# Optimization experiments

Hardware: AMD Instinct MI355X
Metric: run time of the kernel (lower is better)

## Reference

```python
import jax, jax.numpy as jnp
import numpy as np

D_MODEL = 1024
NUM_HEADS = 16
EPS = 1e-5


def _layernorm(x, gamma, beta):
    mu = jnp.mean(x, axis=-1, keepdims=True)
    var = jnp.mean(jnp.square(x - mu), axis=-1, keepdims=True)
    return (x - mu) * jax.lax.rsqrt(var + EPS) * gamma + beta


def setup_inputs() -> dict:
    key = jax.random.key(0)
    ks = jax.random.split(key, 8)
    B, S, D = 4, 2048, D_MODEL
    xav = (6.0 / (D + D)) ** 0.5  # xavier_uniform bound for square D x D
    inp = {
        "q": jax.random.normal(ks[0], (B, S, D), dtype=jnp.float32),
        "k": jax.random.normal(ks[1], (B, S, D), dtype=jnp.float32),
        "v": jax.random.normal(ks[2], (B, S, D), dtype=jnp.float32),
        "Wq": jax.random.uniform(ks[3], (D, D), jnp.float32, -xav, xav),
        "Wk": jax.random.uniform(ks[4], (D, D), jnp.float32, -xav, xav),
        "Wv": jax.random.uniform(ks[5], (D, D), jnp.float32, -xav, xav),
        "Wo": jax.random.uniform(ks[6], (D, D), jnp.float32, -xav, xav),
        "bo": jnp.zeros((D,), jnp.float32),
        "q_gamma": jnp.ones((D,), jnp.float32),
        "q_beta": jnp.zeros((D,), jnp.float32),
        "k_gamma": jnp.ones((D,), jnp.float32),
        "k_beta": jnp.zeros((D,), jnp.float32),
    }
    return inp


def reference(q, k, v, Wq, Wk, Wv, Wo, bo, q_gamma, q_beta, k_gamma, k_beta):
    B, S, D = q.shape
    H = NUM_HEADS
    scale = 1.0 / (D ** 0.5)  # NOTE: 1/sqrt(d_model), as in the source
    qp = _layernorm(q @ Wq, q_gamma, q_beta)  # LN over full d_model, pre-split
    kp = _layernorm(k @ Wk, k_gamma, k_beta)
    vp = v @ Wv
    qh = qp.reshape(B, S, H, D // H)  # [B,S,H,hd]
    kh = kp.reshape(B, S, H, D // H)
    vh = vp.reshape(B, S, H, D // H)
    attn = jnp.einsum("bqhd,bkhd->bhqk", qh, kh) * scale
    attn = jax.nn.softmax(attn, axis=-1)
    x = jnp.einsum("bhqk,bkhd->bqhd", attn, vh).reshape(B, S, D)
    return x @ Wo + bo
```

## Files before the change

kernel.cpp:

```cpp
#include <hip/hip_runtime.h>
#include <hip/hip_bf16.h>

typedef unsigned short u16;
typedef __attribute__((ext_vector_type(8))) short bf16x8;
typedef __attribute__((ext_vector_type(4))) float f32x4;
typedef __attribute__((ext_vector_type(16))) float f32x16;
typedef __attribute__((ext_vector_type(4))) unsigned short u16x4;
typedef __attribute__((ext_vector_type(4))) unsigned int u32x4;
typedef __attribute__((ext_vector_type(2))) int i32x2;

__device__ __forceinline__ u16 f2b(float f) {
    __hip_bfloat16 h = __float2bfloat16(f);
    u16 r; __builtin_memcpy(&r, &h, 2); return r;
}
__device__ __forceinline__ float bf2f(u16 u) {
    return __uint_as_float(((unsigned)u) << 16);
}
__device__ __forceinline__ void gload16(const void* g, void* l) {
    __builtin_amdgcn_global_load_lds(
        (const __attribute__((address_space(1))) unsigned int*)g,
        (__attribute__((address_space(3))) unsigned int*)l, 16, 0, 0);
}
__device__ __forceinline__ float fexp2(float x) {
    return __builtin_amdgcn_exp2f(x);
}
__device__ __forceinline__ unsigned cvtpk(float lo, float hi) {
    unsigned d;
    asm("v_cvt_pk_bf16_f32 %0, %1, %2" : "=v"(d) : "v"(lo), "v"(hi));
    return d;
}
__device__ __forceinline__ bf16x8 mk_pa(float a0, float a1, float a2, float a3,
                                        float b0, float b1, float b2, float b3) {
    int A0 = (int)cvtpk(a0, a1), A1 = (int)cvtpk(a2, a3);
    int B0 = (int)cvtpk(b0, b1), B1 = (int)cvtpk(b2, b3);
    i32x2 r0 = __builtin_amdgcn_permlane32_swap(A0, B0, false, false);
    i32x2 r1 = __builtin_amdgcn_permlane32_swap(A1, B1, false, false);
    u32x4 fw = { (unsigned)r0[0], (unsigned)r1[0], (unsigned)r0[1], (unsigned)r1[1] };
    return __builtin_bit_cast(bf16x8, fw);
}

__global__ __launch_bounds__(256)
void cvt_kernel(const float* __restrict__ in, u16* __restrict__ out) {
    size_t i = ((size_t)blockIdx.x * 256 + threadIdx.x) * 8;
    f32x4 a = *(const f32x4*)(in + i);
    f32x4 b = *(const f32x4*)(in + i + 4);
    u16x4 p0 = { f2b(a[0]), f2b(a[1]), f2b(a[2]), f2b(a[3]) };
    u16x4 p1 = { f2b(b[0]), f2b(b[1]), f2b(b[2]), f2b(b[3]) };
    *(u16x4*)(out + i) = p0;
    *(u16x4*)(out + i + 4) = p1;
}

__global__ __launch_bounds__(256)
void wt_kernel(const float* __restrict__ Wq, const float* __restrict__ Wk,
               const float* __restrict__ Wv, const float* __restrict__ Wo,
               u16* __restrict__ Wt) {
    const float* W = blockIdx.z == 0 ? Wq : blockIdx.z == 1 ? Wk : blockIdx.z == 2 ? Wv : Wo;
    u16* Out = Wt + (size_t)blockIdx.z * (1024 * 1024);
    __shared__ float T[64][65];
    const int t = threadIdx.x;
    const int r0 = blockIdx.y * 64, c0 = blockIdx.x * 64;
#pragma unroll
    for (int e = 0; e < 4; ++e) {
        int row = e * 16 + (t >> 4), c4 = (t & 15) * 4;
        f32x4 v = *(const f32x4*)(W + (r0 + row) * 1024 + c0 + c4);
        T[row][c4] = v[0]; T[row][c4 + 1] = v[1]; T[row][c4 + 2] = v[2]; T[row][c4 + 3] = v[3];
    }
    __syncthreads();
#pragma unroll
    for (int e = 0; e < 4; ++e) {
        int orow = e * 16 + (t >> 4), oc4 = (t & 15) * 4;
        u16x4 pk = { f2b(T[oc4][orow]), f2b(T[oc4 + 1][orow]),
                     f2b(T[oc4 + 2][orow]), f2b(T[oc4 + 3][orow]) };
        *(u16x4*)(Out + (c0 + orow) * 1024 + r0 + oc4) = pk;
    }
}

template <int BIAS>
__global__ __launch_bounds__(256)
void gemm_kernel(const u16* __restrict__ Ab, const u16* __restrict__ Bt,
                 u16* __restrict__ Cb, float* __restrict__ Cf,
                 const float* __restrict__ bias) {
    constexpr int K = 1024;
    __shared__ u16 As[128 * 64];
    __shared__ u16 Bs[128 * 64];
    const int tid = threadIdx.x;
    const int lane = tid & 63, w = tid >> 6;
    const int wr = w >> 1, wc = w & 1;
    const int c = lane & 15, g = lane >> 4;
    const int m0 = blockIdx.y * 128, n0 = blockIdx.x * 128;
    const int sr = lane >> 3, sc = (lane & 7) * 8;
    f32x4 acc[4][4] = {};
    for (int kt = 0; kt < 16; ++kt) {
        const int k0 = kt * 64;
#pragma unroll
        for (int i = 0; i < 4; ++i) {
            int row = 32 * w + 8 * i;
            gload16(Ab + (size_t)(m0 + row + sr) * K + k0 + sc, &As[row * 64]);
            gload16(Bt + (size_t)(n0 + row + sr) * K + k0 + sc, &Bs[row * 64]);
        }
        __syncthreads();
#pragma unroll
        for (int kk = 0; kk < 2; ++kk) {
            bf16x8 af[4], bfr[4];
#pragma unroll
            for (int m = 0; m < 4; ++m)
                af[m] = *(const bf16x8*)&As[(wr * 64 + m * 16 + c) * 64 + kk * 32 + 8 * g];
#pragma unroll
            for (int n = 0; n < 4; ++n)
                bfr[n] = *(const bf16x8*)&Bs[(wc * 64 + n * 16 + c) * 64 + kk * 32 + 8 * g];
#pragma unroll
            for (int m = 0; m < 4; ++m)
#pragma unroll
                for (int n = 0; n < 4; ++n)
                    acc[m][n] = __builtin_amdgcn_mfma_f32_16x16x32_bf16(af[m], bfr[n], acc[m][n], 0, 0, 0);
        }
        __syncthreads();
    }
#pragma unroll
    for (int n = 0; n < 4; ++n) {
        int col = n0 + wc * 64 + n * 16 + c;
        float bv = BIAS ? bias[col] : 0.0f;
#pragma unroll
        for (int m = 0; m < 4; ++m) {
            int row0 = m0 + wr * 64 + m * 16 + 4 * g;
#pragma unroll
            for (int r = 0; r < 4; ++r) {
                if (BIAS) Cf[(row0 + r) * 1024 + col] = acc[m][n][r] + bv;
                else      Cb[(row0 + r) * 1024 + col] = f2b(acc[m][n][r]);
            }
        }
    }
}

__global__ __launch_bounds__(256)
void ln_kernel(const u16* __restrict__ P, const float* __restrict__ gamma,
               const float* __restrict__ beta, float mul, u16* __restrict__ Out) {
    const int row = blockIdx.x;
    const int tid = threadIdx.x;
    const int lane = tid & 63, w = tid >> 6;
    u16x4 xr = *(const u16x4*)(P + row * 1024 + tid * 4);
    float x0 = bf2f(xr[0]), x1 = bf2f(xr[1]), x2 = bf2f(xr[2]), x3 = bf2f(xr[3]);
    float s = x0 + x1 + x2 + x3;
    float sq = x0 * x0 + x1 * x1 + x2 * x2 + x3 * x3;
#pragma unroll
    for (int m = 1; m < 64; m <<= 1) { s += __shfl_xor(s, m); sq += __shfl_xor(sq, m); }
    __shared__ float red[8];
    if (lane == 0) { red[w] = s; red[4 + w] = sq; }
    __syncthreads();
    float st = red[0] + red[1] + red[2] + red[3];
    float sqt = red[4] + red[5] + red[6] + red[7];
    float mu = st * (1.0f / 1024.0f);
    float var = sqt * (1.0f / 1024.0f) - mu * mu;
    float rs = rsqrtf(var + 1e-5f);
    f32x4 gm = *(const f32x4*)(gamma + tid * 4);
    f32x4 bt = *(const f32x4*)(beta + tid * 4);
    float xs[4] = {x0, x1, x2, x3};
    u16x4 pk;
#pragma unroll
    for (int j = 0; j < 4; ++j)
        pk[j] = f2b(((xs[j] - mu) * rs * gm[j] + bt[j]) * mul);
    const int b = row >> 11, sI = row & 2047;
    const int col = tid * 4, hh = col >> 6, d = col & 63;
    *(u16x4*)(Out + (((b * 16 + hh) * 2048 + sI) << 6) + d) = pk;
}

__global__ __launch_bounds__(256)
void vt_kernel(const u16* __restrict__ P, u16* __restrict__ Vt) {
    __shared__ u16 T[64][72];
    const int t = threadIdx.x;
    const int bh = blockIdx.y, s0 = blockIdx.x * 64;
    const int b = bh >> 4, h = bh & 15;
#pragma unroll
    for (int e = 0; e < 4; ++e) {
        int row = e * 16 + (t >> 4), c4 = (t & 15) * 4;
        u16x4 v = *(const u16x4*)(P + (b * 2048 + s0 + row) * 1024 + h * 64 + c4);
        *(u16x4*)&T[row][c4] = v;
    }
    __syncthreads();
#pragma unroll
    for (int e = 0; e < 4; ++e) {
        int dd = e * 16 + (t >> 4), s4 = (t & 15) * 4;
        u16x4 pk = { T[s4][dd], T[s4 + 1][dd], T[s4 + 2][dd], T[s4 + 3][dd] };
        *(u16x4*)(Vt + ((size_t)bh * 64 + dd) * 2048 + s0 + s4) = pk;
    }
}

__global__ __launch_bounds__(256, 4)
void attn_kernel(const u16* __restrict__ Qa, const u16* __restrict__ Ka,
                 const u16* __restrict__ Vt, u16* __restrict__ Xa) {
    __shared__ u16 Ks[2][4096];
    __shared__ u16 Vs[2][4096];
    const int tid = threadIdx.x;
    const int lane = tid & 63, w = tid >> 6;
    const int col = lane & 31, h = lane >> 5;
    const int bid = blockIdx.x;
    const int bh = (bid & 7) * 8 + ((bid >> 3) & 7);
    const int q0 = (bid >> 6) * 128;
    const int b = bh >> 4, hd = bh & 15;
    const int qb = q0 + w * 32;
    const int sw = (col & 7) << 4;

    const u16* qptr = Qa + ((size_t)bh * 2048 + qb + col) * 64;
    bf16x8 qf[4];
#pragma unroll
    for (int s = 0; s < 4; ++s)
        qf[s] = *(const bf16x8*)(qptr + 16 * s + 8 * h);

    const int sr = lane >> 3;
    const int scg = ((lane & 7) ^ sr) * 8;
    const u16* kA = Ka + ((size_t)bh * 2048 + sr) * 64 + scg;
    const u16* vA = Vt + ((size_t)bh * 64 + sr) * 2048 + scg;

    f32x16 o0 = {}, o1 = {};
    float li = 0.f;

#pragma unroll
    for (int j = 0; j < 2; ++j) {
        const int m = 2 * w + j;
        gload16(kA + (size_t)(8 * m) * 64, &Ks[0][8 * m * 64]);
        gload16(vA + (size_t)(8 * m) * 2048, &Vs[0][8 * m * 64]);
    }
    __syncthreads();

    int cur = 0;
    for (int t = 0; t < 32; ++t) {
        const int tn = (t + 1) & 31;
#pragma unroll
        for (int j = 0; j < 2; ++j) {
            const int m = 2 * w + j;
            gload16(kA + (size_t)(tn * 64 + 8 * m) * 64, &Ks[cur ^ 1][8 * m * 64]);
            gload16(vA + (size_t)(8 * m) * 2048 + tn * 64, &Vs[cur ^ 1][8 * m * 64]);
        }

        const char* kbase = (const char*)&Ks[cur][0];
        f32x16 sacc0 = {}, sacc1 = {};
        __builtin_amdgcn_s_setprio(1);
#pragma unroll
        for (int s = 0; s < 4; ++s) {
            bf16x8 kf0 = *(const bf16x8*)(kbase + (col) * 128       + ((32 * s + 16 * h) ^ sw));
            bf16x8 kf1 = *(const bf16x8*)(kbase + (32 + col) * 128  + ((32 * s + 16 * h) ^ sw));
            sacc0 = __builtin_amdgcn_mfma_f32_32x32x16_bf16(kf0, qf[s], sacc0, 0, 0, 0);
            sacc1 = __builtin_amdgcn_mfma_f32_32x32x16_bf16(kf1, qf[s], sacc1, 0, 0, 0);
        }
        __builtin_amdgcn_s_setprio(0);

        f32x16 p0, p1;
#pragma unroll
        for (int r = 0; r < 16; ++r) { p0[r] = fexp2(sacc0[r]); }
#pragma unroll
        for (int r = 0; r < 16; ++r) { p1[r] = fexp2(sacc1[r]); }
#pragma unroll
        for (int r = 0; r < 16; ++r) { li += p0[r] + p1[r]; }

        bf16x8 pa0 = mk_pa(p0[0], p0[1], p0[2], p0[3], p0[4], p0[5], p0[6], p0[7]);
        bf16x8 pa1 = mk_pa(p0[8], p0[9], p0[10], p0[11], p0[12], p0[13], p0[14], p0[15]);
        bf16x8 pa2 = mk_pa(p1[0], p1[1], p1[2], p1[3], p1[4], p1[5], p1[6], p1[7]);
        bf16x8 pa3 = mk_pa(p1[8], p1[9], p1[10], p1[11], p1[12], p1[13], p1[14], p1[15]);

        const char* vb = (const char*)&Vs[cur][0];
        __builtin_amdgcn_s_setprio(1);
#pragma unroll
        for (int sg = 0; sg < 4; ++sg) {
            bf16x8 pf = sg == 0 ? pa0 : sg == 1 ? pa1 : sg == 2 ? pa2 : pa3;
            const int cb = (32 * sg + 16 * h) ^ sw;
            bf16x8 vf0 = *(const bf16x8*)(vb + (col) * 128      + cb);
            bf16x8 vf1 = *(const bf16x8*)(vb + (32 + col) * 128 + cb);
            o0 = __builtin_amdgcn_mfma_f32_32x32x16_bf16(pf, vf0, o0, 0, 0, 0);
            o1 = __builtin_amdgcn_mfma_f32_32x32x16_bf16(pf, vf1, o1, 0, 0, 0);
        }
        __builtin_amdgcn_s_setprio(0);

        __syncthreads();
        cur ^= 1;
    }

    li += __shfl_xor(li, 32);
    float inv = 1.0f / li;
#pragma unroll
    for (int reg = 0; reg < 16; ++reg) {
        const int crow = (reg & 3) + 8 * (reg >> 2) + 4 * h;
        float ivr = __shfl(inv, crow);
        const int row = qb + crow;
        u16* xp = Xa + ((size_t)b * 2048 + row) * 1024 + hd * 64;
        xp[col] = f2b(o0[reg] * ivr);
        xp[32 + col] = f2b(o1[reg] * ivr);
    }
}

extern "C" void kernel_launch(void* const* d_in, const int* in_sizes, int n_in,
                              void* d_out, int out_size, void* d_ws, size_t ws_size,
                              hipStream_t stream) {
    const float* q   = (const float*)d_in[0];
    const float* k   = (const float*)d_in[1];
    const float* v   = (const float*)d_in[2];
    const float* Wq  = (const float*)d_in[3];
    const float* Wk  = (const float*)d_in[4];
    const float* Wv  = (const float*)d_in[5];
    const float* Wo  = (const float*)d_in[6];
    const float* bo  = (const float*)d_in[7];
    const float* qg  = (const float*)d_in[8];
    const float* qbt = (const float*)d_in[9];
    const float* kg  = (const float*)d_in[10];
    const float* kbt = (const float*)d_in[11];

    char* ws = (char*)d_ws;
    u16* Wt = (u16*)(ws);
    u16* Pb = (u16*)(ws + 8388608);
    u16* Qa = (u16*)(ws + 25165824);
    u16* Ka = (u16*)(ws + 41943040);
    u16* Vt = (u16*)(ws + 58720256);
    u16* Ib = (u16*)(ws + 75497472);
    u16* Xa = Pb;

    const float MUL_Q = 0.04508422002778f;

    wt_kernel<<<dim3(16, 16, 4), 256, 0, stream>>>(Wq, Wk, Wv, Wo, Wt);

    cvt_kernel<<<4096, 256, 0, stream>>>(q, Ib);
    gemm_kernel<0><<<dim3(8, 64), 256, 0, stream>>>(Ib, Wt, Pb, nullptr, nullptr);
    ln_kernel<<<8192, 256, 0, stream>>>(Pb, qg, qbt, MUL_Q, Qa);

    cvt_kernel<<<4096, 256, 0, stream>>>(k, Ib);
    gemm_kernel<0><<<dim3(8, 64), 256, 0, stream>>>(Ib, Wt + 1048576, Pb, nullptr, nullptr);
    ln_kernel<<<8192, 256, 0, stream>>>(Pb, kg, kbt, 1.0f, Ka);

    cvt_kernel<<<4096, 256, 0, stream>>>(v, Ib);
    gemm_kernel<0><<<dim3(8, 64), 256, 0, stream>>>(Ib, Wt + 2097152, Pb, nullptr, nullptr);
    vt_kernel<<<dim3(32, 64), 256, 0, stream>>>(Pb, Vt);

    attn_kernel<<<1024, 256, 0, stream>>>(Qa, Ka, Vt, Xa);

    gemm_kernel<1><<<dim3(8, 64), 256, 0, stream>>>((const u16*)Xa, Wt + 3145728, nullptr, (float*)d_out, bo);
}
```

Measured before the change: 253.7 us.

## Batch Q/K/V conversion, projection GEMMs and layernorms into grid-z launches

Merges the three per-input convert, projection GEMM and layernorm launches into single launches indexed by blockIdx.z, using a larger workspace so all three projections live in separate buffers. Each projection GEMM grid alone is 512 blocks, which may underfill the GPU; a combined 1536-block grid fills more compute units and removes several launch gaps. It needs more workspace and keeps the old sequential path as a fallback when the workspace is too small.

```diff
diff --git a/kernel.cpp b/kernel.cpp
--- a/kernel.cpp
+++ b/kernel.cpp
@@ -51,6 +51,21 @@
 }
 
 __global__ __launch_bounds__(256)
+void cvt3_kernel(const float* __restrict__ q, const float* __restrict__ k,
+                 const float* __restrict__ v, u16* __restrict__ out3) {
+    const int z = blockIdx.z;
+    const float* in = z == 0 ? q : z == 1 ? k : v;
+    u16* out = out3 + (size_t)z * 8388608;
+    size_t i = ((size_t)blockIdx.x * 256 + threadIdx.x) * 8;
+    f32x4 a = *(const f32x4*)(in + i);
+    f32x4 b = *(const f32x4*)(in + i + 4);
+    u16x4 p0 = { f2b(a[0]), f2b(a[1]), f2b(a[2]), f2b(a[3]) };
+    u16x4 p1 = { f2b(b[0]), f2b(b[1]), f2b(b[2]), f2b(b[3]) };
+    *(u16x4*)(out + i) = p0;
+    *(u16x4*)(out + i + 4) = p1;
+}
+
+__global__ __launch_bounds__(256)
 void wt_kernel(const float* __restrict__ Wq, const float* __restrict__ Wk,
                const float* __restrict__ Wv, const float* __restrict__ Wo,
                u16* __restrict__ Wt) {
@@ -76,18 +91,17 @@
 }
 
 template <int BIAS>
-__global__ __launch_bounds__(256)
-void gemm_kernel(const u16* __restrict__ Ab, const u16* __restrict__ Bt,
-                 u16* __restrict__ Cb, float* __restrict__ Cf,
-                 const float* __restrict__ bias) {
+__device__ __forceinline__ void gemm_body(const u16* __restrict__ Ab,
+                                          const u16* __restrict__ Bt,
+                                          u16* __restrict__ Cb, float* __restrict__ Cf,
+                                          const float* __restrict__ bias,
+                                          u16* As, u16* Bs, int bx, int by) {
     constexpr int K = 1024;
-    __shared__ u16 As[128 * 64];
-    __shared__ u16 Bs[128 * 64];
     const int tid = threadIdx.x;
     const int lane = tid & 63, w = tid >> 6;
     const int wr = w >> 1, wc = w & 1;
     const int c = lane & 15, g = lane >> 4;
-    const int m0 = blockIdx.y * 128, n0 = blockIdx.x * 128;
+    const int m0 = by * 128, n0 = bx * 128;
     const int sr = lane >> 3, sc = (lane & 7) * 8;
     f32x4 acc[4][4] = {};
     for (int kt = 0; kt < 16; ++kt) {
@@ -132,9 +146,31 @@
     }
 }
 
-__global__ __launch_bounds__(256)
-void ln_kernel(const u16* __restrict__ P, const float* __restrict__ gamma,
-               const float* __restrict__ beta, float mul, u16* __restrict__ Out) {
+template <int BIAS>
+__global__ __launch_bounds__(256)
+void gemm_kernel(const u16* __restrict__ Ab, const u16* __restrict__ Bt,
+                 u16* __restrict__ Cb, float* __restrict__ Cf,
+                 const float* __restrict__ bias) {
+    __shared__ u16 As[128 * 64];
+    __shared__ u16 Bs[128 * 64];
+    gemm_body<BIAS>(Ab, Bt, Cb, Cf, bias, As, Bs, blockIdx.x, blockIdx.y);
+}
+
+__global__ __launch_bounds__(256)
+void gemm3_kernel(const u16* __restrict__ A3, const u16* __restrict__ Wt,
+                  u16* __restrict__ C3) {
+    __shared__ u16 As[128 * 64];
+    __shared__ u16 Bs[128 * 64];
+    const int z = blockIdx.z;
+    gemm_body<0>(A3 + (size_t)z * 8388608, Wt + (size_t)z * 1048576,
+                 C3 + (size_t)z * 8388608, nullptr, nullptr, As, Bs,
+                 blockIdx.x, blockIdx.y);
+}
+
+__device__ __forceinline__ void ln_body(const u16* __restrict__ P,
+                                        const float* __restrict__ gamma,
+                                        const float* __restrict__ beta,
+                                        float mul, u16* __restrict__ Out) {
     const int row = blockIdx.x;
     const int tid = threadIdx.x;
     const int lane = tid & 63, w = tid >> 6;
@@ -162,6 +198,22 @@
     const int b = row >> 11, sI = row & 2047;
     const int col = tid * 4, hh = col >> 6, d = col & 63;
     *(u16x4*)(Out + (((b * 16 + hh) * 2048 + sI) << 6) + d) = pk;
+}
+
+__global__ __launch_bounds__(256)
+void ln_kernel(const u16* __restrict__ P, const float* __restrict__ gamma,
+               const float* __restrict__ beta, float mul, u16* __restrict__ Out) {
+    ln_body(P, gamma, beta, mul, Out);
+}
+
+__global__ __launch_bounds__(256)
+void ln2_kernel(const u16* __restrict__ P3,
+                const float* __restrict__ qg, const float* __restrict__ qb,
+                const float* __restrict__ kg, const float* __restrict__ kb,
+                u16* __restrict__ Qa, u16* __restrict__ Ka, float mulq) {
+    const int z = blockIdx.z;
+    ln_body(P3 + (size_t)z * 8388608, z == 0 ? qg : kg, z == 0 ? qb : kb,
+            z == 0 ? mulq : 1.0f, z == 0 ? Qa : Ka);
 }
 
 __global__ __launch_bounds__(256)
@@ -304,31 +356,44 @@
     const float* kbt = (const float*)d_in[11];
 
     char* ws = (char*)d_ws;
-    u16* Wt = (u16*)(ws);
-    u16* Pb = (u16*)(ws + 8388608);
-    u16* Qa = (u16*)(ws + 25165824);
-    u16* Ka = (u16*)(ws + 41943040);
-    u16* Vt = (u16*)(ws + 58720256);
-    u16* Ib = (u16*)(ws + 75497472);
-    u16* Xa = Pb;
-
     const float MUL_Q = 0.04508422002778f;
 
-    wt_kernel<<<dim3(16, 16, 4), 256, 0, stream>>>(Wq, Wk, Wv, Wo, Wt);
-
-    cvt_kernel<<<4096, 256, 0, stream>>>(q, Ib);
-    gemm_kernel<0><<<dim3(8, 64), 256, 0, stream>>>(Ib, Wt, Pb, nullptr, nullptr);
-    ln_kernel<<<8192, 256, 0, stream>>>(Pb, qg, qbt, MUL_Q, Qa);
-
-    cvt_kernel<<<4096, 256, 0, stream>>>(k, Ib);
-    gemm_kernel<0><<<dim3(8, 64), 256, 0, stream>>>(Ib, Wt + 1048576, Pb, nullptr, nullptr);
-    ln_kernel<<<8192, 256, 0, stream>>>(Pb, kg, kbt, 1.0f, Ka);
-
-    cvt_kernel<<<4096, 256, 0, stream>>>(v, Ib);
-    gemm_kernel<0><<<dim3(8, 64), 256, 0, stream>>>(Ib, Wt + 2097152, Pb, nullptr, nullptr);
-    vt_kernel<<<dim3(32, 64), 256, 0, stream>>>(Pb, Vt);
-
-    attn_kernel<<<1024, 256, 0, stream>>>(Qa, Ka, Vt, Xa);
-
-    gemm_kernel<1><<<dim3(8, 64), 256, 0, stream>>>((const u16*)Xa, Wt + 3145728, nullptr, (float*)d_out, bo);
-}
+    if (ws_size >= 109051904ULL) {
+        u16* Wt  = (u16*)(ws);
+        u16* Ib3 = (u16*)(ws + 8388608);
+        u16* Pb3 = (u16*)(ws + 58720256);
+        u16* Qa  = (u16*)(ws + 8388608);
+        u16* Ka  = (u16*)(ws + 25165824);
+        u16* Vt  = (u16*)(ws + 41943040);
+        u16* Xa  = Pb3;
+
+        wt_kernel<<<dim3(16, 16, 4), 256, 0, stream>>>(Wq, Wk, Wv, Wo, Wt);
+        cvt3_kernel<<<dim3(4096, 1, 3), 256, 0, stream>>>(q, k, v, Ib3);
+        gemm3_kernel<<<dim3(8, 64, 3), 256, 0, stream>>>(Ib3, Wt, Pb3);
+        ln2_kernel<<<dim3(8192, 1, 2), 256, 0, stream>>>(Pb3, qg, qbt, kg, kbt, Qa, Ka, MUL_Q);
+        vt_kernel<<<dim3(32, 64), 256, 0, stream>>>(Pb3 + 2 * 8388608, Vt);
+        attn_kernel<<<1024, 256, 0, stream>>>(Qa, Ka, Vt, Xa);
+        gemm_kernel<1><<<dim3(8, 64), 256, 0, stream>>>((const u16*)Xa, Wt + 3145728, nullptr, (float*)d_out, bo);
+    } else {
+        u16* Wt = (u16*)(ws);
+        u16* Pb = (u16*)(ws + 8388608);
+        u16* Qa = (u16*)(ws + 25165824);
+        u16* Ka = (u16*)(ws + 41943040);
+        u16* Vt = (u16*)(ws + 58720256);
+        u16* Ib = (u16*)(ws + 75497472);
+        u16* Xa = Pb;
+
+        wt_kernel<<<dim3(16, 16, 4), 256, 0, stream>>>(Wq, Wk, Wv, Wo, Wt);
+        cvt_kernel<<<4096, 256, 0, stream>>>(q, Ib);
+        gemm_kernel<0><<<dim3(8, 64), 256, 0, stream>>>(Ib, Wt, Pb, nullptr, nullptr);
+        ln_kernel<<<8192, 256, 0, stream>>>(Pb, qg, qbt, MUL_Q, Qa);
+        cvt_kernel<<<4096, 256, 0, stream>>>(k, Ib);
+        gemm_kernel<0><<<dim3(8, 64), 256, 0, stream>>>(Ib, Wt + 1048576, Pb, nullptr, nullptr);
+        ln_kernel<<<8192, 256, 0, stream>>>(Pb, kg, kbt, 1.0f, Ka);
+        cvt_kernel<<<4096, 256, 0, stream>>>(v, Ib);
+        gemm_kernel<0><<<dim3(8, 64), 256, 0, stream>>>(Ib, Wt + 2097152, Pb, nullptr, nullptr);
+        vt_kernel<<<dim3(32, 64), 256, 0, stream>>>(Pb, Vt);
+        attn_kernel<<<1024, 256, 0, stream>>>(Qa, Ka, Vt, Xa);
+        gemm_kernel<1><<<dim3(8, 64), 256, 0, stream>>>((const u16*)Xa, Wt + 3145728, nullptr, (float*)d_out, bo);
+    }
+}
```

Result: faster. 242.2 us (-4.5%).
